# Kernel optimization log

Measured on AMD Instinct MI355X. Metric: run time of the kernel, lower is better.

The kernel has to match this reference:

```python
import jax, jax.numpy as jnp
import numpy as np

EPS = 1e-12

def _normalize(v):
    n = jnp.linalg.norm(v, axis=-1, keepdims=True)
    return v / jnp.maximum(n, EPS)

def _bgs(J):
    # J: [b, N, D, 3, 2] -> rotation matrices R [b, N, D, 3, 3]
    b1 = _normalize(J[..., :, 0])
    a2 = J[..., :, 1]
    dot = jnp.sum(b1 * a2, axis=-1, keepdims=True)
    b2 = _normalize(a2 - dot * b1)
    b3 = jnp.cross(b1, b2)
    return jnp.stack([b1, b2, b3], axis=-1)  # columns b1,b2,b3

def setup_inputs() -> dict:
    key = jax.random.key(0)
    k1, k2, k3, k4, k5 = jax.random.split(key, 5)
    B, N, D, OUT = 16, 4096, 64, 64
    X = jax.random.normal(k1, (B, N, D, 3), dtype=jnp.float32)
    J = jax.random.normal(k2, (B, N, D, 3, 2), dtype=jnp.float32)
    A = jax.random.normal(k3, (OUT, D), dtype=jnp.float32)
    Bm = jax.random.normal(k4, (OUT, D), dtype=jnp.float32)
    C = jax.random.normal(k5, (OUT, D), dtype=jnp.float32)
    return {"X": X, "J": J, "A": A, "Bm": Bm, "C": C}

def reference(X, J, A, Bm, C):
    R = _bgs(J)  # [b, N, D, 3, 3]
    # RT_i . X == column i of R dotted with X -> scalar per channel
    RTX = jnp.einsum('bndij,bndi->bndj', R, X)  # [b, N, D, 3], j-th entry = RT_j X
    rt0 = RTX[..., 0:1]
    rt1 = RTX[..., 1:2]
    rt2 = RTX[..., 2:3]
    col0 = R[..., :, 0]
    col1 = R[..., :, 1]
    col2 = R[..., :, 2]
    # a_term (after adding b_term, as in original forward)
    a_term = col1 * rt1 + col2 * rt2 + col2 * rt1 - col1 * rt2  # [b, N, D, 3]
    c_term = col0 * rt0
    Y = jnp.einsum('fe,bnei->bnfi', A, a_term) + jnp.einsum('fe,bnei->bnfi', C, c_term)
    Y = jnp.einsum('fe,bnei->bnfi', Bm, Y)
    return Y
```

## Files before the change

kernel.cpp:

```cpp
#include <hip/hip_runtime.h>


typedef __bf16 bf16x8 __attribute__((ext_vector_type(8)));
typedef float floatx4 __attribute__((ext_vector_type(4)));

#define RSW 68

__global__ __launch_bounds__(256) void prep_kernel(const float* __restrict__ A,
                                                   const float* __restrict__ Bm,
                                                   const float* __restrict__ C,
                                                   __bf16* __restrict__ acat) {
    int tid = blockIdx.x * 256 + threadIdx.x;
    int f = tid >> 6;
    int e = tid & 63;
    float m = 0.f, m2 = 0.f;
    #pragma unroll 8
    for (int k = 0; k < 64; ++k) {
        float b = Bm[f * 64 + k];
        m  = fmaf(b, A[k * 64 + e], m);
        m2 = fmaf(b, C[k * 64 + e], m2);
    }
    acat[f * 128 + 2 * e]     = (__bf16)m;
    acat[f * 128 + 2 * e + 1] = (__bf16)m2;
}

static __device__ __forceinline__ unsigned pk(float a, float c) {
    unsigned short ua = __builtin_bit_cast(unsigned short, (__bf16)a);
    unsigned short uc = __builtin_bit_cast(unsigned short, (__bf16)c);
    return ((unsigned)uc << 16) | ua;
}

__global__ __launch_bounds__(256, 5) void main_kernel(const float* __restrict__ X,
                                                      const float* __restrict__ J,
                                                      const __bf16* __restrict__ acat,
                                                      float* __restrict__ out) {
    __shared__ __align__(16) float buf[4][1632];

    const int wave = threadIdx.x >> 6;
    const int lane = threadIdx.x & 63;
    const int l15  = lane & 15;
    const int quad = lane >> 4;
    const int pbase = blockIdx.x * 32 + wave * 8;

    unsigned* zw = (unsigned*)buf[wave];

    #pragma unroll 4
    for (int pi = 0; pi < 8; ++pi) {
        const size_t p = (size_t)(pbase + pi);
        const float2* jp = (const float2*)(J + p * 384) + lane * 3;
        float2 ja = jp[0], jb = jp[1], jc = jp[2];
        const float* xp = X + p * 192 + lane * 3;
        float xx = xp[0], xy = xp[1], xz = xp[2];

        float a0x = ja.x, a0y = jb.x, a0z = jc.x;
        float a1x = ja.y, a1y = jb.y, a1z = jc.y;

        float n0 = sqrtf(a0x * a0x + a0y * a0y + a0z * a0z);
        float r0 = 1.0f / fmaxf(n0, 1e-12f);
        float b1x = a0x * r0, b1y = a0y * r0, b1z = a0z * r0;

        float d  = b1x * a1x + b1y * a1y + b1z * a1z;
        float ux = a1x - d * b1x, uy = a1y - d * b1y, uz = a1z - d * b1z;
        float n2 = sqrtf(ux * ux + uy * uy + uz * uz);
        float r2 = 1.0f / fmaxf(n2, 1e-12f);
        float b2x = ux * r2, b2y = uy * r2, b2z = uz * r2;

        float b3x = b1y * b2z - b1z * b2y;
        float b3y = b1z * b2x - b1x * b2z;
        float b3z = b1x * b2y - b1y * b2x;

        float rt0 = b1x * xx + b1y * xy + b1z * xz;
        float rt1 = b2x * xx + b2y * xy + b2z * xz;
        float rt2 = b3x * xx + b3y * xy + b3z * xz;

        float s = rt1 - rt2, t = rt1 + rt2;

        unsigned* zr = zw + (pi * 3) * RSW;
        zr[lane]           = pk(b2x * s + b3x * t, b1x * rt0);
        zr[RSW + lane]     = pk(b2y * s + b3y * t, b1y * rt0);
        zr[2 * RSW + lane] = pk(b2z * s + b3z * t, b1z * rt0);
    }

    bf16x8 afrag[4][4];
    #pragma unroll
    for (int mt = 0; mt < 4; ++mt)
        #pragma unroll
        for (int kc = 0; kc < 4; ++kc)
            afrag[mt][kc] = *(const bf16x8*)(acat + (mt * 16 + l15) * 128 + kc * 32 + quad * 8);

    __asm__ volatile("s_waitcnt lgkmcnt(0)" ::: "memory");

    floatx4 acc[4][2];
    #pragma unroll
    for (int mt = 0; mt < 4; ++mt)
        #pragma unroll
        for (int nt = 0; nt < 2; ++nt)
            acc[mt][nt] = (floatx4){0.f, 0.f, 0.f, 0.f};

    #pragma unroll
    for (int kc = 0; kc < 4; ++kc) {
        #pragma unroll
        for (int nt = 0; nt < 2; ++nt) {
            int row = nt * 16 + l15;
            row = row > 23 ? 23 : row;
            bf16x8 b = *(const bf16x8*)((const __bf16*)zw + row * 136 + kc * 32 + quad * 8);
            #pragma unroll
            for (int mt = 0; mt < 4; ++mt)
                acc[mt][nt] = __builtin_amdgcn_mfma_f32_16x16x32_bf16(
                    afrag[mt][kc], b, acc[mt][nt], 0, 0, 0);
        }
    }

    __asm__ volatile("s_waitcnt lgkmcnt(0)" ::: "memory");

    float* dl = buf[wave];
    #pragma unroll
    for (int mt = 0; mt < 4; ++mt) {
        #pragma unroll
        for (int nt = 0; nt < 2; ++nt) {
            int n = nt * 16 + l15;
            if (n < 24) {
                int pl = (n * 21846) >> 16;
                int i  = n - pl * 3;
                float* dst = dl + pl * 196 + i;
                #pragma unroll
                for (int r = 0; r < 4; ++r) {
                    int f = mt * 16 + quad * 4 + r;
                    dst[f * 3] = acc[mt][nt][r];
                }
            }
        }
    }

    __asm__ volatile("s_waitcnt lgkmcnt(0)" ::: "memory");

    floatx4* og = (floatx4*)(out + (size_t)pbase * 192);
    #pragma unroll
    for (int t = 0; t < 6; ++t) {
        int g  = t * 64 + lane;
        int pg = (g * 1366) >> 16;
        int o  = g - pg * 48;
        og[g] = *(const floatx4*)(dl + pg * 196 + o * 4);
    }
}

extern "C" void kernel_launch(void* const* d_in, const int* in_sizes, int n_in,
                              void* d_out, int out_size, void* d_ws, size_t ws_size,
                              hipStream_t stream) {
    const float* X  = (const float*)d_in[0];
    const float* J  = (const float*)d_in[1];
    const float* A  = (const float*)d_in[2];
    const float* Bm = (const float*)d_in[3];
    const float* C  = (const float*)d_in[4];
    float* out = (float*)d_out;
    __bf16* acat = (__bf16*)d_ws;

    prep_kernel<<<16, 256, 0, stream>>>(A, Bm, C, acat);

    main_kernel<<<2048, 256, 0, stream>>>(X, J, acat, out);
}
```

Before: 219.8 us.

## Stage J and X through LDS with coalesced vector loads, halve points per wave

Each wave now loads its J and X rows with fully coalesced 16-byte vector loads into LDS, then reads per-lane triples from shared memory, in place of strided 8-byte and 4-byte global loads per lane. Points per wave drop from 8 to 4, so the MFMA N-tile shrinks to one 16-column tile holding 12 valid columns, and the grid doubles. The change targets global-load inefficiency on a memory-bound kernel. The cost is more LDS per block, lower occupancy (launch bounds go from 5 to 3 blocks), and more wasted MFMA columns.

```diff
diff --git a/kernel.cpp b/kernel.cpp
--- a/kernel.cpp
+++ b/kernel.cpp
@@ -30,27 +30,48 @@
     return ((unsigned)uc << 16) | ua;
 }
 
-__global__ __launch_bounds__(256, 5) void main_kernel(const float* __restrict__ X,
+__global__ __launch_bounds__(256, 3) void main_kernel(const float* __restrict__ X,
                                                       const float* __restrict__ J,
                                                       const __bf16* __restrict__ acat,
                                                       float* __restrict__ out) {
-    __shared__ __align__(16) float buf[4][1632];
+    __shared__ __align__(16) float buf[4][3120];
 
     const int wave = threadIdx.x >> 6;
     const int lane = threadIdx.x & 63;
     const int l15  = lane & 15;
     const int quad = lane >> 4;
-    const int pbase = blockIdx.x * 32 + wave * 8;
+    const int pbase = blockIdx.x * 16 + wave * 4;
 
-    unsigned* zw = (unsigned*)buf[wave];
+    float* stg = buf[wave];
 
-    #pragma unroll 4
-    for (int pi = 0; pi < 8; ++pi) {
-        const size_t p = (size_t)(pbase + pi);
-        const float2* jp = (const float2*)(J + p * 384) + lane * 3;
-        float2 ja = jp[0], jb = jp[1], jc = jp[2];
-        const float* xp = X + p * 192 + lane * 3;
-        float xx = xp[0], xy = xp[1], xz = xp[2];
+    {
+        const floatx4* jg = (const floatx4*)(J + (size_t)pbase * 384);
+        const floatx4* xg = (const floatx4*)(X + (size_t)pbase * 192);
+        floatx4 jt[6], xt[3];
+        #pragma unroll
+        for (int t = 0; t < 6; ++t) jt[t] = jg[t * 64 + lane];
+        #pragma unroll
+        for (int t = 0; t < 3; ++t) xt[t] = xg[t * 64 + lane];
+        floatx4* sj = (floatx4*)stg;
+        floatx4* sx = (floatx4*)(stg + 1536);
+        #pragma unroll
+        for (int t = 0; t < 6; ++t) sj[t * 64 + lane] = jt[t];
+        #pragma unroll
+        for (int t = 0; t < 3; ++t) sx[t * 64 + lane] = xt[t];
+    }
+
+    __asm__ volatile("s_waitcnt lgkmcnt(0)" ::: "memory");
+
+    unsigned* zw = (unsigned*)(stg + 2304);
+
+    #pragma unroll
+    for (int pi = 0; pi < 4; ++pi) {
+        const float* jst = stg + pi * 384 + lane * 6;
+        float2 ja = *(const float2*)(jst);
+        float2 jb = *(const float2*)(jst + 2);
+        float2 jc = *(const float2*)(jst + 4);
+        const float* xst = stg + 1536 + pi * 192 + lane * 3;
+        float xx = xst[0], xy = xst[1], xz = xst[2];
 
         float a0x = ja.x, a0y = jb.x, a0z = jc.x;
         float a1x = ja.y, a1y = jb.y, a1z = jc.y;
@@ -90,44 +111,33 @@
 
     __asm__ volatile("s_waitcnt lgkmcnt(0)" ::: "memory");
 
-    floatx4 acc[4][2];
+    floatx4 acc[4];
     #pragma unroll
-    for (int mt = 0; mt < 4; ++mt)
-        #pragma unroll
-        for (int nt = 0; nt < 2; ++nt)
-            acc[mt][nt] = (floatx4){0.f, 0.f, 0.f, 0.f};
+    for (int mt = 0; mt < 4; ++mt) acc[mt] = (floatx4){0.f, 0.f, 0.f, 0.f};
 
+    int row = l15 > 11 ? 11 : l15;
     #pragma unroll
     for (int kc = 0; kc < 4; ++kc) {
+        bf16x8 b = *(const bf16x8*)((const __bf16*)zw + row * 136 + kc * 32 + quad * 8);
         #pragma unroll
-        for (int nt = 0; nt < 2; ++nt) {
-            int row = nt * 16 + l15;
-            row = row > 23 ? 23 : row;
-            bf16x8 b = *(const bf16x8*)((const __bf16*)zw + row * 136 + kc * 32 + quad * 8);
-            #pragma unroll
-            for (int mt = 0; mt < 4; ++mt)
-                acc[mt][nt] = __builtin_amdgcn_mfma_f32_16x16x32_bf16(
-                    afrag[mt][kc], b, acc[mt][nt], 0, 0, 0);
-        }
+        for (int mt = 0; mt < 4; ++mt)
+            acc[mt] = __builtin_amdgcn_mfma_f32_16x16x32_bf16(afrag[mt][kc], b, acc[mt], 0, 0, 0);
     }
 
     __asm__ volatile("s_waitcnt lgkmcnt(0)" ::: "memory");
 
-    float* dl = buf[wave];
+    float* dl = stg;
     #pragma unroll
     for (int mt = 0; mt < 4; ++mt) {
-        #pragma unroll
-        for (int nt = 0; nt < 2; ++nt) {
-            int n = nt * 16 + l15;
-            if (n < 24) {
-                int pl = (n * 21846) >> 16;
-                int i  = n - pl * 3;
-                float* dst = dl + pl * 196 + i;
-                #pragma unroll
-                for (int r = 0; r < 4; ++r) {
-                    int f = mt * 16 + quad * 4 + r;
-                    dst[f * 3] = acc[mt][nt][r];
-                }
+        int n = l15;
+        if (n < 12) {
+            int pl = (n * 21846) >> 16;
+            int i  = n - pl * 3;
+            float* dst = dl + pl * 196 + i;
+            #pragma unroll
+            for (int r = 0; r < 4; ++r) {
+                int f = mt * 16 + quad * 4 + r;
+                dst[f * 3] = acc[mt][r];
             }
         }
     }
@@ -136,7 +146,7 @@
 
     floatx4* og = (floatx4*)(out + (size_t)pbase * 192);
     #pragma unroll
-    for (int t = 0; t < 6; ++t) {
+    for (int t = 0; t < 3; ++t) {
         int g  = t * 64 + lane;
         int pg = (g * 1366) >> 16;
         int o  = g - pg * 48;
@@ -157,5 +167,5 @@
 
     prep_kernel<<<16, 256, 0, stream>>>(A, Bm, C, acat);
 
-    main_kernel<<<2048, 256, 0, stream>>>(X, J, acat, out);
+    main_kernel<<<4096, 256, 0, stream>>>(X, J, acat, out);
 }
```

After: 209.2 us. -4.8%, faster.
